# Optimization experiments

Measured on AMD Instinct MI355X. Metric: run time of the kernel, lower is better.

Reference implementation:

```python
import jax, jax.numpy as jnp
import numpy as np

N = 10000      # nodes
E = 65536      # edges
IN = 16        # in_channels
H = 64         # hidden_channels
ED = 4         # edge_attr_dim
MLP_H = 64     # hidden width of edge-weight MLPs


def _glorot(key, shape):
    fan_in, fan_out = shape[0], shape[1]
    lim = np.sqrt(6.0 / (fan_in + fan_out)).astype(np.float32)
    return jax.random.uniform(key, shape, jnp.float32, -lim, lim)


def setup_inputs() -> dict:
    key = jax.random.key(0)
    ks = jax.random.split(key, 16)
    x = jax.random.normal(ks[0], (N, IN), dtype=jnp.float32)
    edge_index = jax.random.randint(ks[1], (2, E), 0, N, dtype=jnp.int64)
    edge_attr = jax.random.normal(ks[2], (E, ED), dtype=jnp.float32)
    return {
        "x": x,
        "edge_index": edge_index,
        "edge_attr": edge_attr,
        # nn1: Linear(ED,64) -> ReLU -> Linear(64, IN*H)
        "nn1_w1": _glorot(ks[3], (ED, MLP_H)), "nn1_b1": jnp.zeros((MLP_H,), jnp.float32),
        "nn1_w2": _glorot(ks[4], (MLP_H, IN * H)), "nn1_b2": jnp.zeros((IN * H,), jnp.float32),
        "root1": _glorot(ks[5], (IN, H)), "bias1": jnp.zeros((H,), jnp.float32),
        # nn2: Linear(ED,64) -> ReLU -> Linear(64, H*H)
        "nn2_w1": _glorot(ks[6], (ED, MLP_H)), "nn2_b1": jnp.zeros((MLP_H,), jnp.float32),
        "nn2_w2": _glorot(ks[7], (MLP_H, H * H)), "nn2_b2": jnp.zeros((H * H,), jnp.float32),
        "root2": _glorot(ks[8], (H, H)), "bias2": jnp.zeros((H,), jnp.float32),
        # readout MLP
        "lin1_w": _glorot(ks[9], (H, 8)), "lin1_b": jnp.zeros((8,), jnp.float32),
        "lin2_w": _glorot(ks[10], (8, 1)), "lin2_b": jnp.zeros((1,), jnp.float32),
    }


def _nnconv(x, src, dst, edge_attr, w1, b1, w2, b2, root, bias, cin, cout):
    # Edge-conditioned weight generation: MLP(edge_attr) -> [E, cin, cout]
    h = jax.nn.relu(edge_attr @ w1 + b1)
    We = (h @ w2 + b2).reshape(-1, cin, cout)
    # Per-edge matmul: message_e = x[src_e] @ We_e  -> [E, cout]
    msg = jnp.einsum('ei,eio->eo', x[src], We)
    # Scatter mean over destination nodes
    s = jax.ops.segment_sum(msg, dst, num_segments=N)
    cnt = jax.ops.segment_sum(jnp.ones((msg.shape[0],), x.dtype), dst, num_segments=N)
    agg = s / jnp.maximum(cnt, 1.0)[:, None]
    # Root transform + bias (PyG NNConv defaults: root_weight=True, bias=True)
    return agg + x @ root + bias


def reference(x, edge_index, edge_attr,
              nn1_w1, nn1_b1, nn1_w2, nn1_b2, root1, bias1,
              nn2_w1, nn2_b1, nn2_w2, nn2_b2, root2, bias2,
              lin1_w, lin1_b, lin2_w, lin2_b):
    # Dropout layers are identity in eval mode.
    src, dst = edge_index[0], edge_index[1]
    h = jax.nn.relu(_nnconv(x, src, dst, edge_attr,
                            nn1_w1, nn1_b1, nn1_w2, nn1_b2, root1, bias1, IN, H))
    h = jax.nn.relu(_nnconv(h, src, dst, edge_attr,
                            nn2_w1, nn2_b1, nn2_w2, nn2_b2, root2, bias2, H, H))
    h = jax.nn.relu(h @ lin1_w + lin1_b)
    return (h @ lin2_w + lin2_b)[:, 0]  # squeeze(-1) -> [N]
```

## Files before the change

### kernel.cpp

```cpp
#include <hip/hip_runtime.h>
#include <hip/hip_bf16.h>

#define NN 10000
#define EE 65536

using short8  = __attribute__((ext_vector_type(8))) short;
using u16x8   = __attribute__((ext_vector_type(8))) unsigned short;
using float4v = __attribute__((ext_vector_type(4))) float;

__device__ __forceinline__ unsigned short f2b(float f){
  union { float f; unsigned int u; } v; v.f = f;
  unsigned int u = v.u;
  unsigned int r = (u + 0x7fff + ((u >> 16) & 1)) >> 16;
  return (unsigned short)r;
}


__device__ __forceinline__ void do_permB(int idx, const float* __restrict__ w2,
                                         unsigned short* __restrict__ Bt, int cin){
  int K = cin*64;
  int o = idx / K;
  int k = idx - o*K;
  int m = k / cin;
  int i = k - m*cin;
  Bt[idx] = f2b(w2[(size_t)m*(cin*64) + i*64 + o]);
}

__device__ __forceinline__ void do_mlp(int idx, const float* __restrict__ ea,
                                       const float* __restrict__ w1, const float* __restrict__ b1,
                                       float* __restrict__ h){
  int m = idx & 63;
  int e = idx >> 6;
  const float* a = ea + (size_t)e*4;
  float acc = b1[m] + a[0]*w1[m] + a[1]*w1[64+m] + a[2]*w1[128+m] + a[3]*w1[192+m];
  h[idx] = fmaxf(acc, 0.f);
}

__global__ __launch_bounds__(256) void k_prep(const float* __restrict__ ea,
    const float* __restrict__ w1a, const float* __restrict__ b1a, float* __restrict__ h1,
    const float* __restrict__ w1b, const float* __restrict__ b1b, float* __restrict__ h2,
    const float* __restrict__ w2a, unsigned short* __restrict__ Bt1,
    const float* __restrict__ w2b, unsigned short* __restrict__ Bt2,
    int* __restrict__ cnt){
  int b = blockIdx.x;
  int t = threadIdx.x;
  if(b < 40){
    int i = b*256 + t;
    if(i < NN) cnt[i] = 0;
  } else if(b < 296){
    do_permB((b-40)*256 + t, w2a, Bt1, 16);
  } else if(b < 1320){
    do_permB((b-296)*256 + t, w2b, Bt2, 64);
  } else if(b < 17704){
    do_mlp((b-1320)*256 + t, ea, w1a, b1a, h1);
  } else {
    do_mlp((b-17704)*256 + t, ea, w1b, b1b, h2);
  }
}


__global__ void k_hist(const int* __restrict__ dst, int* __restrict__ cnt){
  int e = blockIdx.x*256 + threadIdx.x;
  if(e < EE) atomicAdd(&cnt[dst[e]], 1);
}

__global__ __launch_bounds__(1024) void k_scan(const int* __restrict__ cnt, int* __restrict__ offs, int* __restrict__ cursor){
  const int T = 1024, PER = (NN + T - 1)/T;
  int tid = threadIdx.x;
  int base = tid*PER;
  int local[PER];
  int s = 0;
  #pragma unroll
  for(int j=0;j<PER;j++){
    int i = base+j;
    int v = (i<NN)? cnt[i] : 0;
    local[j] = s;
    s += v;
  }
  int lane = tid & 63, wv = tid >> 6;
  int val = s;
  #pragma unroll
  for(int o=1;o<64;o<<=1){
    int u = __shfl_up(val, o, 64);
    if(lane >= o) val += u;
  }
  __shared__ int wsum[16];
  if(lane==63) wsum[wv] = val;
  __syncthreads();
  if(tid==0){
    int acc=0;
    #pragma unroll
    for(int i=0;i<16;i++){ int t2=wsum[i]; wsum[i]=acc; acc+=t2; }
  }
  __syncthreads();
  int thr_excl = wsum[wv] + (val - s);
  #pragma unroll
  for(int j=0;j<PER;j++){
    int i = base+j;
    if(i<NN){ int e = thr_excl + local[j]; offs[i]=e; cursor[i]=e; }
  }
  if(tid == T-1) offs[NN] = thr_excl + s;
}

__global__ void k_scatter(const int* __restrict__ dst, int* __restrict__ cursor, int* __restrict__ elist){
  int e = blockIdx.x*256 + threadIdx.x;
  if(e < EE){ int p = atomicAdd(&cursor[dst[e]], 1); elist[p] = e; }
}


__global__ __launch_bounds__(64) void k_accK1(const float* __restrict__ x, const int* __restrict__ src,
    const int* __restrict__ offs, const int* __restrict__ elist, const float* __restrict__ h,
    unsigned short* __restrict__ K1, float* __restrict__ XS, int v0){
  int v = v0 + blockIdx.x;
  int L = threadIdx.x;
  int cg = L & 3, mg = L >> 2;
  int i0 = cg << 2;
  __shared__ float sh[2][64];
  float acc[4][4];
  #pragma unroll
  for(int j=0;j<4;j++)
    #pragma unroll
    for(int c=0;c<4;c++) acc[j][c]=0.f;
  float4 xs = make_float4(0.f,0.f,0.f,0.f);
  int p0 = offs[v], p1 = offs[v+1];
  float h_nxt = 0.f;
  float4 x_nxt = make_float4(0.f,0.f,0.f,0.f);
  if(p0 < p1){
    int e = elist[p0];
    h_nxt = h[(size_t)e*64 + L];
    x_nxt = *(const float4*)(x + (size_t)src[e]*16 + i0);
  }
  for(int p=p0;p<p1;p++){
    int buf = (p-p0)&1;
    float4 xv = x_nxt;
    sh[buf][L] = h_nxt;
    __syncthreads();
    if(p+1<p1){
      int e = elist[p+1];
      h_nxt = h[(size_t)e*64 + L];
      x_nxt = *(const float4*)(x + (size_t)src[e]*16 + i0);
    }
    xs.x += xv.x; xs.y += xv.y; xs.z += xv.z; xs.w += xv.w;
    #pragma unroll
    for(int j=0;j<4;j++){
      float hv = sh[buf][mg + 16*j];
      acc[j][0] += hv*xv.x; acc[j][1] += hv*xv.y;
      acc[j][2] += hv*xv.z; acc[j][3] += hv*xv.w;
    }
  }
  unsigned short* Kv = K1 + (size_t)blockIdx.x*1024;
  #pragma unroll
  for(int j=0;j<4;j++){
    int m = mg + 16*j;
    ushort4 u;
    u.x=f2b(acc[j][0]); u.y=f2b(acc[j][1]); u.z=f2b(acc[j][2]); u.w=f2b(acc[j][3]);
    *(ushort4*)(Kv + m*16 + i0) = u;
  }
  if(mg==0) *(float4*)(XS + (size_t)v*64 + i0) = xs;
}


__global__ __launch_bounds__(64) void k_accK2(const float* __restrict__ x1, const int* __restrict__ src,
    const int* __restrict__ offs, const int* __restrict__ elist, const float* __restrict__ h,
    unsigned short* __restrict__ K, float* __restrict__ XS, int v0){
  int v = v0 + blockIdx.x;
  int L = threadIdx.x;
  int cg = L & 7, mg = L >> 3;
  int i0 = cg << 3;
  __shared__ float sh[2][64];
  float acc[8][8];
  #pragma unroll
  for(int j=0;j<8;j++)
    #pragma unroll
    for(int c=0;c<8;c++) acc[j][c]=0.f;
  float4 xs0 = make_float4(0.f,0.f,0.f,0.f);
  float4 xs1 = make_float4(0.f,0.f,0.f,0.f);
  int p0 = offs[v], p1 = offs[v+1];
  float h_nxt = 0.f;
  float4 x_nxt0 = make_float4(0.f,0.f,0.f,0.f);
  float4 x_nxt1 = make_float4(0.f,0.f,0.f,0.f);
  if(p0 < p1){
    int e = elist[p0];
    h_nxt = h[(size_t)e*64 + L];
    const float* xr = x1 + (size_t)src[e]*64 + i0;
    x_nxt0 = *(const float4*)xr;
    x_nxt1 = *(const float4*)(xr+4);
  }
  for(int p=p0;p<p1;p++){
    int buf = (p-p0)&1;
    float4 xv0 = x_nxt0, xv1 = x_nxt1;
    sh[buf][L] = h_nxt;
    __syncthreads();
    if(p+1<p1){
      int e = elist[p+1];
      h_nxt = h[(size_t)e*64 + L];
      const float* xr = x1 + (size_t)src[e]*64 + i0;
      x_nxt0 = *(const float4*)xr;
      x_nxt1 = *(const float4*)(xr+4);
    }
    xs0.x += xv0.x; xs0.y += xv0.y; xs0.z += xv0.z; xs0.w += xv0.w;
    xs1.x += xv1.x; xs1.y += xv1.y; xs1.z += xv1.z; xs1.w += xv1.w;
    float4 h4a = *(float4*)&sh[buf][mg*8];
    float4 h4b = *(float4*)&sh[buf][mg*8+4];
    #pragma unroll
    for(int jj=0;jj<2;jj++){
      float4 h4 = jj? h4b : h4a;
      #pragma unroll
      for(int tq=0;tq<4;tq++){
        int j = jj*4+tq;
        float hv = (tq==0)?h4.x:(tq==1)?h4.y:(tq==2)?h4.z:h4.w;
        acc[j][0] += hv*xv0.x; acc[j][1] += hv*xv0.y;
        acc[j][2] += hv*xv0.z; acc[j][3] += hv*xv0.w;
        acc[j][4] += hv*xv1.x; acc[j][5] += hv*xv1.y;
        acc[j][6] += hv*xv1.z; acc[j][7] += hv*xv1.w;
      }
    }
  }
  unsigned short* Kv = K + (size_t)blockIdx.x*4096;
  #pragma unroll
  for(int j=0;j<8;j++){
    int m = mg*8 + j;
    u16x8 u;
    #pragma unroll
    for(int c=0;c<8;c++) u[c] = f2b(acc[j][c]);
    *(u16x8*)(Kv + m*64 + i0) = u;
  }
  if(mg==0){
    *(float4*)(XS + (size_t)v*64 + i0)     = xs0;
    *(float4*)(XS + (size_t)v*64 + i0 + 4) = xs1;
  }
}


#define GBK 64

__global__ __launch_bounds__(256) void k_gemm(const unsigned short* __restrict__ A,
    const unsigned short* __restrict__ Bt, float* __restrict__ P,
    int rows, int Ktot, int Kc){
  __shared__ unsigned short As[128*72];
  __shared__ unsigned short Bs[64*72];
  int t = threadIdx.x;
  int lane = t & 63;
  int w = t >> 6;
  int row0 = blockIdx.x*128;
  int k0 = blockIdx.y*Kc;

  int srow  = t >> 3;
  int skseg = (t & 7) << 3;

  float4v acc[2][4];
  #pragma unroll
  for(int rt=0;rt<2;rt++)
    #pragma unroll
    for(int ct=0;ct<4;ct++)
      #pragma unroll
      for(int qq=0;qq<4;qq++) acc[rt][ct][qq]=0.f;

  int lrow = lane & 15;
  int lk   = (lane >> 4) << 3;

  short8 a_pf[4], b_pf[2];
  int T = Kc/GBK;

  {
    int kk = k0 + skseg;
    #pragma unroll
    for(int qq=0;qq<4;qq++){
      int gr = row0 + srow + 32*qq;
      short8 z = {0,0,0,0,0,0,0,0};
      a_pf[qq] = (gr<rows)? *(const short8*)(A + (size_t)gr*Ktot + kk) : z;
    }
    #pragma unroll
    for(int qq=0;qq<2;qq++){
      int o = srow + 32*qq;
      b_pf[qq] = *(const short8*)(Bt + (size_t)o*Ktot + kk);
    }
  }

  for(int tt=0; tt<T; tt++){
    __syncthreads();
    #pragma unroll
    for(int qq=0;qq<4;qq++)
      *(short8*)(As + (srow + 32*qq)*72 + skseg) = a_pf[qq];
    #pragma unroll
    for(int qq=0;qq<2;qq++)
      *(short8*)(Bs + (srow + 32*qq)*72 + skseg) = b_pf[qq];
    __syncthreads();
    if(tt+1 < T){
      int kk = k0 + (tt+1)*GBK + skseg;
      #pragma unroll
      for(int qq=0;qq<4;qq++){
        int gr = row0 + srow + 32*qq;
        short8 z = {0,0,0,0,0,0,0,0};
        a_pf[qq] = (gr<rows)? *(const short8*)(A + (size_t)gr*Ktot + kk) : z;
      }
      #pragma unroll
      for(int qq=0;qq<2;qq++){
        int o = srow + 32*qq;
        b_pf[qq] = *(const short8*)(Bt + (size_t)o*Ktot + kk);
      }
    }
    #pragma unroll
    for(int k32=0;k32<2;k32++){
      int kf = k32*32 + lk;
      short8 a0 = *(short8*)(As + (w*32      + lrow)*72 + kf);
      short8 a1 = *(short8*)(As + (w*32 + 16 + lrow)*72 + kf);
      #pragma unroll
      for(int ct=0;ct<4;ct++){
        short8 b = *(short8*)(Bs + (ct*16 + lrow)*72 + kf);
        acc[0][ct] = __builtin_amdgcn_mfma_f32_16x16x32_bf16(a0, b, acc[0][ct], 0,0,0);
        acc[1][ct] = __builtin_amdgcn_mfma_f32_16x16x32_bf16(a1, b, acc[1][ct], 0,0,0);
      }
    }
  }
  size_t base = (size_t)blockIdx.y*rows*64;
  int quad = lane >> 4;
  #pragma unroll
  for(int rt=0;rt<2;rt++){
    #pragma unroll
    for(int ct=0;ct<4;ct++){
      int c = ct*16 + lrow;
      #pragma unroll
      for(int reg=0;reg<4;reg++){
        int r = row0 + w*32 + rt*16 + quad*4 + reg;
        if(r < rows) P[base + (size_t)r*64 + c] = acc[rt][ct][reg];
      }
    }
  }
}


template<int CIN, int SPLIT>
__global__ __launch_bounds__(256) void k_reduce_ep(const float* __restrict__ P, int rows, int v0,
    const float* __restrict__ XS, const float* __restrict__ b2, const float* __restrict__ xprev,
    const float* __restrict__ root, const float* __restrict__ bias, const int* __restrict__ offs,
    float* __restrict__ out){
  int idx = blockIdx.x*256 + threadIdx.x;
  if(idx >= rows*16) return;
  int r = idx >> 4, og = (idx & 15) << 2;
  int v = v0 + r;

  float4 s = make_float4(0.f,0.f,0.f,0.f);
  #pragma unroll
  for(int z=0; z<SPLIT; z++){
    float4 p = *(const float4*)(P + ((size_t)z*rows + r)*64 + og);
    s.x += p.x; s.y += p.y; s.z += p.z; s.w += p.w;
  }
  #pragma unroll
  for(int i=0;i<CIN;i++){
    float xsv = XS[(size_t)v*64 + i];
    float4 b = *(const float4*)(b2 + i*64 + og);
    s.x += xsv*b.x; s.y += xsv*b.y; s.z += xsv*b.z; s.w += xsv*b.w;
  }
  float4 rt = make_float4(0.f,0.f,0.f,0.f);
  #pragma unroll
  for(int i=0;i<CIN;i++){
    float xv = xprev[(size_t)v*CIN + i];
    float4 wv = *(const float4*)(root + i*64 + og);
    rt.x += xv*wv.x; rt.y += xv*wv.y; rt.z += xv*wv.z; rt.w += xv*wv.w;
  }
  float c = (float)(offs[v+1]-offs[v]); c = fmaxf(c, 1.f);
  float inv = 1.f/c;
  float4 bi = *(const float4*)(bias + og);
  float4 o;
  o.x = fmaxf(s.x*inv + rt.x + bi.x, 0.f);
  o.y = fmaxf(s.y*inv + rt.y + bi.y, 0.f);
  o.z = fmaxf(s.z*inv + rt.z + bi.z, 0.f);
  o.w = fmaxf(s.w*inv + rt.w + bi.w, 0.f);
  *(float4*)(out + (size_t)v*64 + og) = o;
}


template<int SPLIT>
__global__ __launch_bounds__(256) void k_red2_ro(const float* __restrict__ P, int rows,
    const float* __restrict__ XS, const float* __restrict__ b2, const float* __restrict__ x1,
    const float* __restrict__ root, const float* __restrict__ bias, const int* __restrict__ offs,
    const float* __restrict__ lw1, const float* __restrict__ lb1,
    const float* __restrict__ lw2, const float* __restrict__ lb2,
    float* __restrict__ out){
  __shared__ float row[16][68];
  __shared__ float hjs[16][8];
  int tid = threadIdx.x;
  int idx = blockIdx.x*256 + tid;
  int r = idx >> 4, og = (idx & 15) << 2;
  int n = tid >> 4;
  int nbase = blockIdx.x*16;
  int ninblk = rows - nbase; if(ninblk > 16) ninblk = 16;

  float4 o = make_float4(0.f,0.f,0.f,0.f);
  if(r < rows){
    float4 s = make_float4(0.f,0.f,0.f,0.f);
    #pragma unroll
    for(int z=0; z<SPLIT; z++){
      float4 p = *(const float4*)(P + ((size_t)z*rows + r)*64 + og);
      s.x += p.x; s.y += p.y; s.z += p.z; s.w += p.w;
    }
    #pragma unroll
    for(int i=0;i<64;i++){
      float xsv = XS[(size_t)r*64 + i];
      float4 b = *(const float4*)(b2 + i*64 + og);
      s.x += xsv*b.x; s.y += xsv*b.y; s.z += xsv*b.z; s.w += xsv*b.w;
    }
    float4 rt = make_float4(0.f,0.f,0.f,0.f);
    #pragma unroll
    for(int i=0;i<64;i++){
      float xv = x1[(size_t)r*64 + i];
      float4 wv = *(const float4*)(root + i*64 + og);
      rt.x += xv*wv.x; rt.y += xv*wv.y; rt.z += xv*wv.z; rt.w += xv*wv.w;
    }
    float c = (float)(offs[r+1]-offs[r]); c = fmaxf(c, 1.f);
    float inv = 1.f/c;
    float4 bi = *(const float4*)(bias + og);
    o.x = fmaxf(s.x*inv + rt.x + bi.x, 0.f);
    o.y = fmaxf(s.y*inv + rt.y + bi.y, 0.f);
    o.z = fmaxf(s.z*inv + rt.z + bi.z, 0.f);
    o.w = fmaxf(s.w*inv + rt.w + bi.w, 0.f);
  }
  *(float4*)&row[n][og] = o;
  __syncthreads();
  if(tid < 128){
    int n2 = tid >> 3, j = tid & 7;
    if(n2 < ninblk){
      float a = lb1[j];
      #pragma unroll
      for(int i=0;i<64;i++) a += row[n2][i]*lw1[i*8+j];
      hjs[n2][j] = fmaxf(a, 0.f)*lw2[j];
    }
  }
  __syncthreads();
  if(tid < 16 && tid < ninblk){
    float s = lb2[0];
    #pragma unroll
    for(int j=0;j<8;j++) s += hjs[tid][j];
    out[nbase + tid] = s;
  }
}


__global__ void k_readout(const float* __restrict__ x2, const float* __restrict__ lw1,
                          const float* __restrict__ lb1, const float* __restrict__ lw2,
                          const float* __restrict__ lb2, float* __restrict__ out){
  int v = blockIdx.x*256 + threadIdx.x;
  if(v >= NN) return;
  float accj[8];
  #pragma unroll
  for(int j=0;j<8;j++) accj[j] = lb1[j];
  const float* xr = x2 + (size_t)v*64;
  #pragma unroll 16
  for(int i=0;i<64;i++){
    float xv = xr[i];
    #pragma unroll
    for(int j=0;j<8;j++) accj[j] += xv*lw1[i*8+j];
  }
  float o = lb2[0];
  #pragma unroll
  for(int j=0;j<8;j++) o += fmaxf(accj[j],0.f)*lw2[j];
  out[v] = o;
}


extern "C" void kernel_launch(void* const* d_in, const int* in_sizes, int n_in,
                              void* d_out, int out_size, void* d_ws, size_t ws_size,
                              hipStream_t stream) {
  const float* x      = (const float*)d_in[0];
  const int*   ei     = (const int*)d_in[1];
  const float* ea     = (const float*)d_in[2];
  const float* nn1_w1 = (const float*)d_in[3];
  const float* nn1_b1 = (const float*)d_in[4];
  const float* nn1_w2 = (const float*)d_in[5];
  const float* nn1_b2 = (const float*)d_in[6];
  const float* root1  = (const float*)d_in[7];
  const float* bias1  = (const float*)d_in[8];
  const float* nn2_w1 = (const float*)d_in[9];
  const float* nn2_b1 = (const float*)d_in[10];
  const float* nn2_w2 = (const float*)d_in[11];
  const float* nn2_b2 = (const float*)d_in[12];
  const float* root2  = (const float*)d_in[13];
  const float* bias2  = (const float*)d_in[14];
  const float* lin1_w = (const float*)d_in[15];
  const float* lin1_b = (const float*)d_in[16];
  const float* lin2_w = (const float*)d_in[17];
  const float* lin2_b = (const float*)d_in[18];
  float* out = (float*)d_out;

  const int* srcIdx = ei;
  const int* dstIdx = ei + EE;

  char* w = (char*)d_ws;
  size_t off = 0;
  auto alloc = [&](size_t bytes)->void*{
    void* p = w + off;
    off = (off + bytes + 255) & ~(size_t)255;
    return p;
  };
  int*            cnt    = (int*)           alloc((size_t)NN*4);
  int*            offs   = (int*)           alloc((size_t)(NN+1)*4);
  int*            cursor = (int*)           alloc((size_t)NN*4);
  int*            elist  = (int*)           alloc((size_t)EE*4);
  float*          h1     = (float*)         alloc((size_t)EE*64*4);
  float*          h2     = (float*)         alloc((size_t)EE*64*4);
  float*          XS     = (float*)         alloc((size_t)NN*64*4);
  float*          x1     = (float*)         alloc((size_t)NN*64*4);
  unsigned short* Bt1    = (unsigned short*)alloc((size_t)64*1024*2);
  unsigned short* Bt2    = (unsigned short*)alloc((size_t)64*4096*2);
  size_t fixedBytes = off;
  size_t R = (ws_size > fixedBytes) ? (ws_size - fixedBytes) : 0;

  const int S1 = 4, S2 = 8;
  size_t needSingle = (size_t)NN*4096*2 + (size_t)S2*NN*64*4;
  bool single = (R >= needSingle + 4096);

  k_prep<<<34088, 256, 0, stream>>>(ea, nn1_w1, nn1_b1, h1, nn2_w1, nn2_b1, h2,
                                    nn1_w2, Bt1, nn2_w2, Bt2, cnt);
  k_hist   <<<(EE+255)/256, 256, 0, stream>>>(dstIdx, cnt);
  k_scan   <<<1, 1024, 0, stream>>>(cnt, offs, cursor);
  k_scatter<<<(EE+255)/256, 256, 0, stream>>>(dstIdx, cursor, elist);

  if(single){
    unsigned short* Kbuf = (unsigned short*)(w + off);
    float* P = (float*)(w + off + (size_t)NN*4096*2);

    k_accK1<<<NN, 64, 0, stream>>>(x, srcIdx, offs, elist, h1, Kbuf, XS, 0);
    {
      dim3 g((NN+127)/128, S1);
      k_gemm<<<g, 256, 0, stream>>>(Kbuf, Bt1, P, NN, 1024, 1024/S1);
    }
    k_reduce_ep<16,S1><<<(NN*16+255)/256, 256, 0, stream>>>(P, NN, 0, XS, nn1_b2, x,
                                                             root1, bias1, offs, x1);
    k_accK2<<<NN, 64, 0, stream>>>(x1, srcIdx, offs, elist, h2, Kbuf, XS, 0);
    {
      dim3 g((NN+127)/128, S2);
      k_gemm<<<g, 256, 0, stream>>>(Kbuf, Bt2, P, NN, 4096, 4096/S2);
    }
    k_red2_ro<S2><<<(NN+15)/16, 256, 0, stream>>>(P, NN, XS, nn2_b2, x1, root2, bias2, offs,
                                                   lin1_w, lin1_b, lin2_w, lin2_b, out);
  } else {
    float* x2b = (float*)alloc((size_t)NN*64*4);
    R = (ws_size > off) ? (ws_size - off) : 0;
    long long C2 = (long long)(R / (4096*2 + S2*64*4));
    long long C1 = (long long)(R / (1024*2 + S1*64*4));
    if(C2 > NN) C2 = NN; if(C1 > NN) C1 = NN;
    if(C2 < 128) C2 = 128; if(C1 < 128) C1 = 128;
    unsigned short* Kbuf = (unsigned short*)(w + off);
    {
      float* P = (float*)(w + off + (size_t)C1*1024*2);
      for(long long v0=0; v0<NN; v0+=C1){
        int rows = (int)((NN - v0 < C1) ? (NN - v0) : C1);
        k_accK1<<<rows, 64, 0, stream>>>(x, srcIdx, offs, elist, h1, Kbuf, XS, (int)v0);
        dim3 g((rows+127)/128, S1);
        k_gemm<<<g, 256, 0, stream>>>(Kbuf, Bt1, P, rows, 1024, 1024/S1);
        k_reduce_ep<16,S1><<<(rows*16+255)/256, 256, 0, stream>>>(P, rows, (int)v0, XS, nn1_b2, x,
                                                                   root1, bias1, offs, x1);
      }
    }
    {
      float* P = (float*)(w + off + (size_t)C2*4096*2);
      for(long long v0=0; v0<NN; v0+=C2){
        int rows = (int)((NN - v0 < C2) ? (NN - v0) : C2);
        k_accK2<<<rows, 64, 0, stream>>>(x1, srcIdx, offs, elist, h2, Kbuf, XS, (int)v0);
        dim3 g((rows+127)/128, S2);
        k_gemm<<<g, 256, 0, stream>>>(Kbuf, Bt2, P, rows, 4096, 4096/S2);
        k_reduce_ep<64,S2><<<(rows*16+255)/256, 256, 0, stream>>>(P, rows, (int)v0, XS, nn2_b2, x1,
                                                                   root2, bias2, offs, x2b);
      }
    }
    k_readout<<<(NN+255)/256, 256, 0, stream>>>(x2b, lin1_w, lin1_b, lin2_w, lin2_b, out);
  }
}
```

Measured before the change: 219.8 us.

## Fuse edge MLP into accumulation kernels and build CSR in one block

Stops materializing the two E×64 hidden-activation buffers h1/h2. The first edge-MLP layer is now computed on the fly inside k_accK1/k_accK2 from a float4 load of edge_attr, which removes about 33 MB of global writes and reads. Histogram, scan and scatter are merged into a single 1024-thread kernel that works on a shared-memory count array, saving launches and global atomics. The trade-off is that CSR construction now runs serially in one workgroup, and the edge order within each node's list still depends on atomic timing.

```diff
diff --git a/kernel.cpp b/kernel.cpp
--- a/kernel.cpp
+++ b/kernel.cpp
@@ -26,54 +26,41 @@
   Bt[idx] = f2b(w2[(size_t)m*(cin*64) + i*64 + o]);
 }
 
-__device__ __forceinline__ void do_mlp(int idx, const float* __restrict__ ea,
-                                       const float* __restrict__ w1, const float* __restrict__ b1,
-                                       float* __restrict__ h){
-  int m = idx & 63;
-  int e = idx >> 6;
-  const float* a = ea + (size_t)e*4;
-  float acc = b1[m] + a[0]*w1[m] + a[1]*w1[64+m] + a[2]*w1[128+m] + a[3]*w1[192+m];
-  h[idx] = fmaxf(acc, 0.f);
-}
-
-__global__ __launch_bounds__(256) void k_prep(const float* __restrict__ ea,
-    const float* __restrict__ w1a, const float* __restrict__ b1a, float* __restrict__ h1,
-    const float* __restrict__ w1b, const float* __restrict__ b1b, float* __restrict__ h2,
+__global__ __launch_bounds__(256) void k_prep(
     const float* __restrict__ w2a, unsigned short* __restrict__ Bt1,
-    const float* __restrict__ w2b, unsigned short* __restrict__ Bt2,
-    int* __restrict__ cnt){
+    const float* __restrict__ w2b, unsigned short* __restrict__ Bt2){
   int b = blockIdx.x;
   int t = threadIdx.x;
-  if(b < 40){
-    int i = b*256 + t;
-    if(i < NN) cnt[i] = 0;
-  } else if(b < 296){
-    do_permB((b-40)*256 + t, w2a, Bt1, 16);
-  } else if(b < 1320){
-    do_permB((b-296)*256 + t, w2b, Bt2, 64);
-  } else if(b < 17704){
-    do_mlp((b-1320)*256 + t, ea, w1a, b1a, h1);
+  if(b < 256){
+    do_permB(b*256 + t, w2a, Bt1, 16);
   } else {
-    do_mlp((b-17704)*256 + t, ea, w1b, b1b, h2);
-  }
-}
-
-
-__global__ void k_hist(const int* __restrict__ dst, int* __restrict__ cnt){
-  int e = blockIdx.x*256 + threadIdx.x;
-  if(e < EE) atomicAdd(&cnt[dst[e]], 1);
-}
-
-__global__ __launch_bounds__(1024) void k_scan(const int* __restrict__ cnt, int* __restrict__ offs, int* __restrict__ cursor){
+    do_permB((b-256)*256 + t, w2b, Bt2, 64);
+  }
+}
+
+
+__global__ __launch_bounds__(1024) void k_csr(const int* __restrict__ dst,
+    int* __restrict__ offs, int* __restrict__ elist){
+  __shared__ int scnt[NN];
+  __shared__ int wsum[16];
   const int T = 1024, PER = (NN + T - 1)/T;
   int tid = threadIdx.x;
+  #pragma unroll
+  for(int j=0;j<PER;j++){
+    int i = tid*PER + j;
+    if(i < NN) scnt[i] = 0;
+  }
+  __syncthreads();
+  for(int e = tid; e < EE; e += T)
+    atomicAdd(&scnt[dst[e]], 1);
+  __syncthreads();
   int base = tid*PER;
   int local[PER];
   int s = 0;
   #pragma unroll
   for(int j=0;j<PER;j++){
     int i = base+j;
-    int v = (i<NN)? cnt[i] : 0;
+    int v = (i<NN)? scnt[i] : 0;
     local[j] = s;
     s += v;
   }
@@ -84,7 +71,6 @@
     int u = __shfl_up(val, o, 64);
     if(lane >= o) val += u;
   }
-  __shared__ int wsum[16];
   if(lane==63) wsum[wv] = val;
   __syncthreads();
   if(tid==0){
@@ -94,27 +80,31 @@
   }
   __syncthreads();
   int thr_excl = wsum[wv] + (val - s);
+  __syncthreads();
   #pragma unroll
   for(int j=0;j<PER;j++){
     int i = base+j;
-    if(i<NN){ int e = thr_excl + local[j]; offs[i]=e; cursor[i]=e; }
+    if(i<NN){ int e = thr_excl + local[j]; offs[i]=e; scnt[i]=e; }
   }
   if(tid == T-1) offs[NN] = thr_excl + s;
-}
-
-__global__ void k_scatter(const int* __restrict__ dst, int* __restrict__ cursor, int* __restrict__ elist){
-  int e = blockIdx.x*256 + threadIdx.x;
-  if(e < EE){ int p = atomicAdd(&cursor[dst[e]], 1); elist[p] = e; }
+  __syncthreads();
+  for(int e = tid; e < EE; e += T){
+    int p = atomicAdd(&scnt[dst[e]], 1);
+    elist[p] = e;
+  }
 }
 
 
 __global__ __launch_bounds__(64) void k_accK1(const float* __restrict__ x, const int* __restrict__ src,
-    const int* __restrict__ offs, const int* __restrict__ elist, const float* __restrict__ h,
+    const int* __restrict__ offs, const int* __restrict__ elist,
+    const float* __restrict__ ea, const float* __restrict__ w1, const float* __restrict__ b1,
     unsigned short* __restrict__ K1, float* __restrict__ XS, int v0){
   int v = v0 + blockIdx.x;
   int L = threadIdx.x;
   int cg = L & 3, mg = L >> 2;
   int i0 = cg << 2;
+  float w1c0 = w1[L], w1c1 = w1[64+L], w1c2 = w1[128+L], w1c3 = w1[192+L];
+  float b1c = b1[L];
   __shared__ float sh[2][64];
   float acc[4][4];
   #pragma unroll
@@ -123,29 +113,31 @@
     for(int c=0;c<4;c++) acc[j][c]=0.f;
   float4 xs = make_float4(0.f,0.f,0.f,0.f);
   int p0 = offs[v], p1 = offs[v+1];
-  float h_nxt = 0.f;
+  float4 a_nxt = make_float4(0.f,0.f,0.f,0.f);
   float4 x_nxt = make_float4(0.f,0.f,0.f,0.f);
   if(p0 < p1){
     int e = elist[p0];
-    h_nxt = h[(size_t)e*64 + L];
+    a_nxt = *(const float4*)(ea + (size_t)e*4);
     x_nxt = *(const float4*)(x + (size_t)src[e]*16 + i0);
   }
   for(int p=p0;p<p1;p++){
     int buf = (p-p0)&1;
     float4 xv = x_nxt;
-    sh[buf][L] = h_nxt;
+    float4 av = a_nxt;
+    float hv = fmaxf(b1c + av.x*w1c0 + av.y*w1c1 + av.z*w1c2 + av.w*w1c3, 0.f);
+    sh[buf][L] = hv;
     __syncthreads();
     if(p+1<p1){
       int e = elist[p+1];
-      h_nxt = h[(size_t)e*64 + L];
+      a_nxt = *(const float4*)(ea + (size_t)e*4);
       x_nxt = *(const float4*)(x + (size_t)src[e]*16 + i0);
     }
     xs.x += xv.x; xs.y += xv.y; xs.z += xv.z; xs.w += xv.w;
     #pragma unroll
     for(int j=0;j<4;j++){
-      float hv = sh[buf][mg + 16*j];
-      acc[j][0] += hv*xv.x; acc[j][1] += hv*xv.y;
-      acc[j][2] += hv*xv.z; acc[j][3] += hv*xv.w;
+      float hm = sh[buf][mg + 16*j];
+      acc[j][0] += hm*xv.x; acc[j][1] += hm*xv.y;
+      acc[j][2] += hm*xv.z; acc[j][3] += hm*xv.w;
     }
   }
   unsigned short* Kv = K1 + (size_t)blockIdx.x*1024;
@@ -161,12 +153,15 @@
 
 
 __global__ __launch_bounds__(64) void k_accK2(const float* __restrict__ x1, const int* __restrict__ src,
-    const int* __restrict__ offs, const int* __restrict__ elist, const float* __restrict__ h,
+    const int* __restrict__ offs, const int* __restrict__ elist,
+    const float* __restrict__ ea, const float* __restrict__ w1, const float* __restrict__ b1,
     unsigned short* __restrict__ K, float* __restrict__ XS, int v0){
   int v = v0 + blockIdx.x;
   int L = threadIdx.x;
   int cg = L & 7, mg = L >> 3;
   int i0 = cg << 3;
+  float w1c0 = w1[L], w1c1 = w1[64+L], w1c2 = w1[128+L], w1c3 = w1[192+L];
+  float b1c = b1[L];
   __shared__ float sh[2][64];
   float acc[8][8];
   #pragma unroll
@@ -176,12 +171,12 @@
   float4 xs0 = make_float4(0.f,0.f,0.f,0.f);
   float4 xs1 = make_float4(0.f,0.f,0.f,0.f);
   int p0 = offs[v], p1 = offs[v+1];
-  float h_nxt = 0.f;
+  float4 a_nxt = make_float4(0.f,0.f,0.f,0.f);
   float4 x_nxt0 = make_float4(0.f,0.f,0.f,0.f);
   float4 x_nxt1 = make_float4(0.f,0.f,0.f,0.f);
   if(p0 < p1){
     int e = elist[p0];
-    h_nxt = h[(size_t)e*64 + L];
+    a_nxt = *(const float4*)(ea + (size_t)e*4);
     const float* xr = x1 + (size_t)src[e]*64 + i0;
     x_nxt0 = *(const float4*)xr;
     x_nxt1 = *(const float4*)(xr+4);
@@ -189,11 +184,13 @@
   for(int p=p0;p<p1;p++){
     int buf = (p-p0)&1;
     float4 xv0 = x_nxt0, xv1 = x_nxt1;
-    sh[buf][L] = h_nxt;
+    float4 av = a_nxt;
+    float hv = fmaxf(b1c + av.x*w1c0 + av.y*w1c1 + av.z*w1c2 + av.w*w1c3, 0.f);
+    sh[buf][L] = hv;
     __syncthreads();
     if(p+1<p1){
       int e = elist[p+1];
-      h_nxt = h[(size_t)e*64 + L];
+      a_nxt = *(const float4*)(ea + (size_t)e*4);
       const float* xr = x1 + (size_t)src[e]*64 + i0;
       x_nxt0 = *(const float4*)xr;
       x_nxt1 = *(const float4*)(xr+4);
@@ -208,11 +205,11 @@
       #pragma unroll
       for(int tq=0;tq<4;tq++){
         int j = jj*4+tq;
-        float hv = (tq==0)?h4.x:(tq==1)?h4.y:(tq==2)?h4.z:h4.w;
-        acc[j][0] += hv*xv0.x; acc[j][1] += hv*xv0.y;
-        acc[j][2] += hv*xv0.z; acc[j][3] += hv*xv0.w;
-        acc[j][4] += hv*xv1.x; acc[j][5] += hv*xv1.y;
-        acc[j][6] += hv*xv1.z; acc[j][7] += hv*xv1.w;
+        float hm = (tq==0)?h4.x:(tq==1)?h4.y:(tq==2)?h4.z:h4.w;
+        acc[j][0] += hm*xv0.x; acc[j][1] += hm*xv0.y;
+        acc[j][2] += hm*xv0.z; acc[j][3] += hm*xv0.w;
+        acc[j][4] += hm*xv1.x; acc[j][5] += hm*xv1.y;
+        acc[j][6] += hm*xv1.z; acc[j][7] += hm*xv1.w;
       }
     }
   }
@@ -493,12 +490,8 @@
     off = (off + bytes + 255) & ~(size_t)255;
     return p;
   };
-  int*            cnt    = (int*)           alloc((size_t)NN*4);
   int*            offs   = (int*)           alloc((size_t)(NN+1)*4);
-  int*            cursor = (int*)           alloc((size_t)NN*4);
   int*            elist  = (int*)           alloc((size_t)EE*4);
-  float*          h1     = (float*)         alloc((size_t)EE*64*4);
-  float*          h2     = (float*)         alloc((size_t)EE*64*4);
   float*          XS     = (float*)         alloc((size_t)NN*64*4);
   float*          x1     = (float*)         alloc((size_t)NN*64*4);
   unsigned short* Bt1    = (unsigned short*)alloc((size_t)64*1024*2);
@@ -510,24 +503,21 @@
   size_t needSingle = (size_t)NN*4096*2 + (size_t)S2*NN*64*4;
   bool single = (R >= needSingle + 4096);
 
-  k_prep<<<34088, 256, 0, stream>>>(ea, nn1_w1, nn1_b1, h1, nn2_w1, nn2_b1, h2,
-                                    nn1_w2, Bt1, nn2_w2, Bt2, cnt);
-  k_hist   <<<(EE+255)/256, 256, 0, stream>>>(dstIdx, cnt);
-  k_scan   <<<1, 1024, 0, stream>>>(cnt, offs, cursor);
-  k_scatter<<<(EE+255)/256, 256, 0, stream>>>(dstIdx, cursor, elist);
+  k_prep<<<1280, 256, 0, stream>>>(nn1_w2, Bt1, nn2_w2, Bt2);
+  k_csr <<<1, 1024, 0, stream>>>(dstIdx, offs, elist);
 
   if(single){
     unsigned short* Kbuf = (unsigned short*)(w + off);
     float* P = (float*)(w + off + (size_t)NN*4096*2);
 
-    k_accK1<<<NN, 64, 0, stream>>>(x, srcIdx, offs, elist, h1, Kbuf, XS, 0);
+    k_accK1<<<NN, 64, 0, stream>>>(x, srcIdx, offs, elist, ea, nn1_w1, nn1_b1, Kbuf, XS, 0);
     {
       dim3 g((NN+127)/128, S1);
       k_gemm<<<g, 256, 0, stream>>>(Kbuf, Bt1, P, NN, 1024, 1024/S1);
     }
     k_reduce_ep<16,S1><<<(NN*16+255)/256, 256, 0, stream>>>(P, NN, 0, XS, nn1_b2, x,
                                                              root1, bias1, offs, x1);
-    k_accK2<<<NN, 64, 0, stream>>>(x1, srcIdx, offs, elist, h2, Kbuf, XS, 0);
+    k_accK2<<<NN, 64, 0, stream>>>(x1, srcIdx, offs, elist, ea, nn2_w1, nn2_b1, Kbuf, XS, 0);
     {
       dim3 g((NN+127)/128, S2);
       k_gemm<<<g, 256, 0, stream>>>(Kbuf, Bt2, P, NN, 4096, 4096/S2);
@@ -546,7 +536,7 @@
       float* P = (float*)(w + off + (size_t)C1*1024*2);
       for(long long v0=0; v0<NN; v0+=C1){
         int rows = (int)((NN - v0 < C1) ? (NN - v0) : C1);
-        k_accK1<<<rows, 64, 0, stream>>>(x, srcIdx, offs, elist, h1, Kbuf, XS, (int)v0);
+        k_accK1<<<rows, 64, 0, stream>>>(x, srcIdx, offs, elist, ea, nn1_w1, nn1_b1, Kbuf, XS, (int)v0);
         dim3 g((rows+127)/128, S1);
         k_gemm<<<g, 256, 0, stream>>>(Kbuf, Bt1, P, rows, 1024, 1024/S1);
         k_reduce_ep<16,S1><<<(rows*16+255)/256, 256, 0, stream>>>(P, rows, (int)v0, XS, nn1_b2, x,
@@ -557,7 +547,7 @@
       float* P = (float*)(w + off + (size_t)C2*4096*2);
       for(long long v0=0; v0<NN; v0+=C2){
         int rows = (int)((NN - v0 < C2) ? (NN - v0) : C2);
-        k_accK2<<<rows, 64, 0, stream>>>(x1, srcIdx, offs, elist, h2, Kbuf, XS, (int)v0);
+        k_accK2<<<rows, 64, 0, stream>>>(x1, srcIdx, offs, elist, ea, nn2_w1, nn2_b1, Kbuf, XS, (int)v0);
         dim3 g((rows+127)/128, S2);
         k_gemm<<<g, 256, 0, stream>>>(Kbuf, Bt2, P, rows, 4096, 4096/S2);
         k_reduce_ep<64,S2><<<(rows*16+255)/256, 256, 0, stream>>>(P, rows, (int)v0, XS, nn2_b2, x1,
```

Result: slower. 253.0 us (+15.1%).
